# Optimization experiments

Measured on AMD Instinct MI355X. Metric: run time of the kernel, lower is better.

The kernel has to match this reference:

```python
import jax, jax.numpy as jnp
import numpy as np

EPS = 1e-12


def t5_layer_norm(x, w):
    # RMS norm without mean subtraction (T5 style)
    var = jnp.mean(x * x, axis=-1, keepdims=True)
    return w * (x * jax.lax.rsqrt(var + EPS))


def gether(h, a_simi, t_simi, adj):
    # h: [B,S,S,D]; a_simi/t_simi: [B,S]; adj: [B,S,S]
    diag = jnp.einsum('bssd->bsd', h)                 # h[b,l,l,:]
    h_adj = jnp.einsum('bld,blk->blkd', diag, adj)    # diag broadcast by adjacency
    h_y = h * t_simi[:, None, :, None]                # t_simi varies along axis 2
    h_x = h * a_simi[:, :, None, None]                # a_simi varies along axis 1
    h_left = jnp.pad(h_y, ((0, 0), (0, 0), (1, 0), (0, 0)))[:, :, :-1, :]
    h_right = jnp.pad(h_y, ((0, 0), (0, 0), (0, 1), (0, 0)))[:, :, 1:, :]
    h_up = jnp.pad(h_x, ((0, 0), (1, 0), (0, 0), (0, 0)))[:, :-1, :, :]
    h_down = jnp.pad(h_x, ((0, 0), (0, 1), (0, 0), (0, 0)))[:, 1:, :, :]
    return h + h_adj + h_left + h_right + h_up + h_down


def setup_inputs() -> dict:
    key = jax.random.key(0)
    ks = jax.random.split(key, 10)
    B, S, D_in, D_out = 8, 96, 768, 256
    table = jax.random.normal(ks[0], (B, S, S, D_in), dtype=jnp.float32)
    a_simi = jax.random.uniform(ks[1], (B, S), dtype=jnp.float32)
    t_simi = jax.random.uniform(ks[2], (B, S), dtype=jnp.float32)
    adj_matrix = jax.random.uniform(ks[3], (B, S, S), dtype=jnp.float32)
    s1 = 1.0 / np.sqrt(D_in)
    W1 = jax.random.uniform(ks[4], (D_in, D_in), jnp.float32, -s1, s1)
    b1 = jax.random.uniform(ks[5], (D_in,), jnp.float32, -s1, s1)
    g1 = jnp.ones((D_in,), jnp.float32)
    W2 = jax.random.uniform(ks[6], (D_in, D_out), jnp.float32, -s1, s1)
    b2 = jax.random.uniform(ks[7], (D_out,), jnp.float32, -s1, s1)
    g2 = jnp.ones((D_out,), jnp.float32)
    return {"table": table, "a_simi": a_simi, "t_simi": t_simi,
            "adj_matrix": adj_matrix, "W1": W1, "b1": b1, "g1": g1,
            "W2": W2, "b2": b2, "g2": g2}


def reference(table, a_simi, t_simi, adj_matrix, W1, b1, g1, W2, b2, g2):
    h0 = table
    h1 = gether(h0, a_simi, t_simi, adj_matrix)
    h1 = jax.nn.relu(t5_layer_norm((h1 + h0) @ W1 + b1, g1))
    h2 = gether(h1, a_simi, t_simi, adj_matrix)
    h2 = jax.nn.relu(t5_layer_norm((h2 + h1) @ W2 + b2, g2))
    return h2
```

## Files before the change

kernel.cpp:

```cpp
#include <hip/hip_runtime.h>

typedef __bf16 bf16;
typedef __bf16 bf16x4 __attribute__((ext_vector_type(4)));
typedef __bf16 bf16x8 __attribute__((ext_vector_type(8)));
typedef float f32x4 __attribute__((ext_vector_type(4)));
typedef float floatx4 __attribute__((ext_vector_type(4)));

#define S 96
#define DIN 768
#define DOUT 256
#define MROWS 73728

__device__ static inline void async16(const bf16* g, bf16* l) {
    __builtin_amdgcn_global_load_lds(
        (const __attribute__((address_space(1))) void*)g,
        (__attribute__((address_space(3))) void*)l,
        16, 0, 0);
}

__global__ __launch_bounds__(256) void k_gether1(
    const float* __restrict__ H, const float* __restrict__ Asim,
    const float* __restrict__ Tsim, const float* __restrict__ Adj,
    bf16* __restrict__ X)
{
    __shared__ float adjs[S];
    __shared__ float ts[S];
    __shared__ float diagf[DIN];
    int b = blockIdx.x / S, l = blockIdx.x % S;
    int tid = threadIdx.x;
    long row0 = (long)(b * S + l) * S;
    if (tid < S) {
        adjs[tid] = Adj[(b * S + l) * S + tid];
        ts[tid]   = Tsim[b * S + tid];
    }
    for (int i = tid; i < DIN / 4; i += 256)
        *(f32x4*)&diagf[i * 4] = *(const f32x4*)&H[(row0 + l) * DIN + i * 4];
    float a_up = (l > 0)     ? Asim[b * S + l - 1] : 0.f;
    float a_dn = (l < S - 1) ? Asim[b * S + l + 1] : 0.f;
    long du = (l > 0)     ? -(long)S * DIN : 0;
    long dd = (l < S - 1) ?  (long)S * DIN : 0;
    __syncthreads();

    for (int it = tid; it < S * (DIN / 4); it += 256) {
        int k = it / (DIN / 4);
        int c = it - k * (DIN / 4);
        const float* hc = H + (row0 + k) * DIN + c * 4;
        float tl = (k > 0)     ? ts[k - 1] : 0.f;
        float tr = (k < S - 1) ? ts[k + 1] : 0.f;
        long  dl = (k > 0)     ? -(long)DIN : 0;
        long  dr = (k < S - 1) ?  (long)DIN : 0;
        f32x4 vc = *(const f32x4*)hc;
        f32x4 vl = *(const f32x4*)(hc + dl);
        f32x4 vr = *(const f32x4*)(hc + dr);
        f32x4 vu = *(const f32x4*)(hc + du);
        f32x4 vd = *(const f32x4*)(hc + dd);
        float aj = adjs[k];
        bf16x4 o;
#pragma unroll
        for (int j = 0; j < 4; ++j) {
            float v = 2.f * vc[j] + aj * diagf[c * 4 + j]
                    + tl * vl[j] + tr * vr[j]
                    + a_up * vu[j] + a_dn * vd[j];
            o[j] = (bf16)v;
        }
        *(bf16x4*)&X[(row0 + k) * DIN + c * 4] = o;
    }
}

__global__ __launch_bounds__(256) void k_gether2(
    const bf16* __restrict__ Y, const float* __restrict__ INV,
    const float* __restrict__ G1, const float* __restrict__ Asim,
    const float* __restrict__ Tsim, const float* __restrict__ Adj,
    bf16* __restrict__ X)
{
    __shared__ float adjs[S];
    __shared__ float ts[S];
    __shared__ float diagf[DIN];
    __shared__ float g1s[DIN];
    int b = blockIdx.x / S, l = blockIdx.x % S;
    int tid = threadIdx.x;
    long row0 = (long)(b * S + l) * S;
    for (int i = tid; i < DIN; i += 256) g1s[i] = G1[i];
    __syncthreads();
    if (tid < S) {
        adjs[tid] = Adj[(b * S + l) * S + tid];
        ts[tid]   = Tsim[b * S + tid];
        float iv = INV[row0 + l];
        bf16x8 yv = *(const bf16x8*)&Y[(row0 + l) * DIN + tid * 8];
#pragma unroll
        for (int j = 0; j < 8; ++j) {
            float v = g1s[tid * 8 + j] * (float)yv[j] * iv;
            diagf[tid * 8 + j] = v > 0.f ? v : 0.f;
        }
    }
    float a_up = (l > 0)     ? Asim[b * S + l - 1] : 0.f;
    float a_dn = (l < S - 1) ? Asim[b * S + l + 1] : 0.f;
    long du = (l > 0)     ? -(long)S * DIN : 0;
    long dd = (l < S - 1) ?  (long)S * DIN : 0;
    int ou = (l > 0) ? -S : 0;
    int od = (l < S - 1) ? S : 0;
    __syncthreads();

    for (int it = tid; it < S * (DIN / 8); it += 256) {
        int k = it / (DIN / 8);
        int c = it - k * (DIN / 8);
        const bf16* yc = Y + (row0 + k) * DIN + c * 8;
        float tl = (k > 0)     ? ts[k - 1] : 0.f;
        float tr = (k < S - 1) ? ts[k + 1] : 0.f;
        int   ol = (k > 0)     ? -1 : 0;
        int   orr = (k < S - 1) ? 1 : 0;
        float ivc = INV[row0 + k];
        float ivl = INV[row0 + k + ol];
        float ivr = INV[row0 + k + orr];
        float ivu = INV[row0 + k + ou];
        float ivd = INV[row0 + k + od];
        bf16x8 vc = *(const bf16x8*)yc;
        bf16x8 vl = *(const bf16x8*)(yc + (long)ol * DIN);
        bf16x8 vr = *(const bf16x8*)(yc + (long)orr * DIN);
        bf16x8 vu = *(const bf16x8*)(yc + du);
        bf16x8 vd = *(const bf16x8*)(yc + dd);
        float aj = adjs[k];
        bf16x8 o;
#pragma unroll
        for (int j = 0; j < 8; ++j) {
            float g = g1s[c * 8 + j];
            float hc_ = g * (float)vc[j] * ivc; hc_ = hc_ > 0.f ? hc_ : 0.f;
            float hl_ = g * (float)vl[j] * ivl; hl_ = hl_ > 0.f ? hl_ : 0.f;
            float hr_ = g * (float)vr[j] * ivr; hr_ = hr_ > 0.f ? hr_ : 0.f;
            float hu_ = g * (float)vu[j] * ivu; hu_ = hu_ > 0.f ? hu_ : 0.f;
            float hd_ = g * (float)vd[j] * ivd; hd_ = hd_ > 0.f ? hd_ : 0.f;
            float v = 2.f * hc_ + aj * diagf[c * 8 + j]
                    + tl * hl_ + tr * hr_ + a_up * hu_ + a_dn * hd_;
            o[j] = (bf16)v;
        }
        *(bf16x8*)&X[(row0 + k) * DIN + c * 8] = o;
    }
}

template <int N, typename OutT>
__global__ __launch_bounds__(256) void k_gemm(
    const bf16* __restrict__ Xm, const bf16* __restrict__ WT,
    const float* __restrict__ bias, OutT* __restrict__ Y,
    float* __restrict__ ssq)
{
    constexpr int K = 768;
    __shared__ __align__(16) bf16 As[128 * 32];
    __shared__ __align__(16) bf16 Bs[128 * 32];
    int t = threadIdx.x;
    int colBase = blockIdx.x * 128;
    int rowBase = blockIdx.y * 128;
    int lane = t & 63, w = t >> 6;
    int quad = lane >> 4, l16 = lane & 15;
    int wr = w >> 1, wc = w & 1;

    floatx4 acc[4][4];
#pragma unroll
    for (int i = 0; i < 4; ++i)
#pragma unroll
        for (int j = 0; j < 4; ++j) acc[i][j] = (floatx4)0.f;

    const bf16* gA = Xm + (size_t)(rowBase + (t >> 2)) * K + (t & 3) * 8;
    const bf16* gB = WT + (size_t)(colBase + (t >> 2)) * K + (t & 3) * 8;
    bf16* ldsA = &As[t * 8];
    bf16* ldsB = &Bs[t * 8];

    for (int kk = 0; kk < K; kk += 32) {
        __syncthreads();
        async16(gA + kk, ldsA);
        async16(gA + kk + 64 * K, ldsA + 2048);
        async16(gB + kk, ldsB);
        async16(gB + kk + 64 * K, ldsB + 2048);
        __syncthreads();
        bf16x8 af[4], bfr[4];
#pragma unroll
        for (int i = 0; i < 4; ++i)
            af[i] = *(const bf16x8*)&As[(wr * 64 + i * 16 + l16) * 32 + quad * 8];
#pragma unroll
        for (int i = 0; i < 4; ++i)
            bfr[i] = *(const bf16x8*)&Bs[(wc * 64 + i * 16 + l16) * 32 + quad * 8];
#pragma unroll
        for (int i = 0; i < 4; ++i)
#pragma unroll
            for (int j = 0; j < 4; ++j)
                acc[i][j] = __builtin_amdgcn_mfma_f32_16x16x32_bf16(
                    af[i], bfr[j], acc[i][j], 0, 0, 0);
    }

    float bv[4];
#pragma unroll
    for (int j = 0; j < 4; ++j)
        bv[j] = bias[colBase + wc * 64 + j * 16 + l16];
#pragma unroll
    for (int i = 0; i < 4; ++i) {
#pragma unroll
        for (int r = 0; r < 4; ++r) {
            int row = rowBase + wr * 64 + i * 16 + quad * 4 + r;
            OutT* yp = Y + (size_t)row * N + colBase + wc * 64 + l16;
            float s = 0.f;
#pragma unroll
            for (int j = 0; j < 4; ++j) {
                float v = acc[i][j][r] + bv[j];
                s += v * v;
                yp[j * 16] = (OutT)v;
            }
            s += __shfl_xor(s, 1);
            s += __shfl_xor(s, 2);
            s += __shfl_xor(s, 4);
            s += __shfl_xor(s, 8);
            if (l16 == 0) atomicAdd(&ssq[row], s);
        }
    }
}

__global__ __launch_bounds__(256) void k_invr(float* ssq, int n, float invD)
{
    int i = blockIdx.x * 256 + threadIdx.x;
    if (i < n) ssq[i] = rsqrtf(ssq[i] * invD + 1e-12f);
}

__global__ __launch_bounds__(256) void k_final(
    const float* __restrict__ Y2, const float* __restrict__ ssq2,
    const float* __restrict__ G2, float* __restrict__ out)
{
    int gidx = blockIdx.x * 256 + threadIdx.x;
    int r = gidx >> 6;
    int c = (gidx & 63) * 4;
    float inv = rsqrtf(ssq2[r] * (1.f / DOUT) + 1e-12f);
    f32x4 yv = *(const f32x4*)&Y2[(size_t)r * DOUT + c];
    f32x4 o;
#pragma unroll
    for (int j = 0; j < 4; ++j) {
        float v = G2[c + j] * yv[j] * inv;
        o[j] = v > 0.f ? v : 0.f;
    }
    *(f32x4*)&out[(size_t)r * DOUT + c] = o;
}

__global__ __launch_bounds__(256) void k_castT(
    const float* __restrict__ in, bf16* __restrict__ out, int R, int C)
{
    int idx = blockIdx.x * 256 + threadIdx.x;
    if (idx < R * C) {
        int c = idx / R, r = idx - c * R;
        out[idx] = (bf16)in[r * C + c];
    }
}

extern "C" void kernel_launch(void* const* d_in, const int* in_sizes, int n_in,
                              void* d_out, int out_size, void* d_ws, size_t ws_size,
                              hipStream_t stream)
{
    const float* table = (const float*)d_in[0];
    const float* asim  = (const float*)d_in[1];
    const float* tsim  = (const float*)d_in[2];
    const float* adj   = (const float*)d_in[3];
    const float* W1    = (const float*)d_in[4];
    const float* b1    = (const float*)d_in[5];
    const float* g1    = (const float*)d_in[6];
    const float* W2    = (const float*)d_in[7];
    const float* b2    = (const float*)d_in[8];
    const float* g2    = (const float*)d_in[9];
    float* out = (float*)d_out;

    char* ws = (char*)d_ws;
    const size_t SZ_X = (size_t)MROWS * DIN * 2;
    bf16*  X    = (bf16*)ws;
    bf16*  Y1   = (bf16*)(ws + SZ_X);
    float* Y2   = (float*)(ws + SZ_X);
    bf16*  W1T  = (bf16*)(ws + 2 * SZ_X);
    bf16*  W2T  = (bf16*)(ws + 2 * SZ_X + 1179648);
    float* ssq1 = (float*)(ws + 2 * SZ_X + 1179648 + 393216);
    float* ssq2 = ssq1 + MROWS;

    hipMemsetAsync(ssq1, 0, (size_t)MROWS * 4 * 2, stream);
    k_castT<<<2304, 256, 0, stream>>>(W1, W1T, DIN, DIN);
    k_castT<<<768, 256, 0, stream>>>(W2, W2T, DIN, DOUT);

    k_gether1<<<8 * S, 256, 0, stream>>>(table, asim, tsim, adj, X);
    k_gemm<DIN, bf16><<<dim3(DIN / 128, MROWS / 128), 256, 0, stream>>>(X, W1T, b1, Y1, ssq1);
    k_invr<<<MROWS / 256, 256, 0, stream>>>(ssq1, MROWS, 1.f / DIN);
    k_gether2<<<8 * S, 256, 0, stream>>>(Y1, ssq1, g1, asim, tsim, adj, X);
    k_gemm<DOUT, float><<<dim3(DOUT / 128, MROWS / 128), 256, 0, stream>>>(X, W2T, b2, Y2, ssq2);
    k_final<<<(MROWS * DOUT / 4) / 256, 256, 0, stream>>>(Y2, ssq2, g2, out);
}
```

Baseline: 700.3 us.

## Restructure gether loops, load GEMM B from global, swizzle LDS, tiled transpose

The gether kernels now give each wavefront whole rows, with a fixed per-lane column unroll, instead of a flat index that needed a divide and modulo. The GEMM drops the LDS staging for the weight tile and loads B fragments straight from global memory (the weights are small and likely cached). It XOR-swizzles the A tile in LDS to cut bank conflicts, swaps the grid axes and adds an occupancy hint to launch bounds. The weight cast-transpose now goes through a padded shared-memory tile so reads and writes are coalesced. The risks are that the swapped grid order may reduce cache reuse of activation tiles across column blocks, and that per-wave global B loads add L2 traffic.

```diff
diff --git a/kernel.cpp b/kernel.cpp
--- a/kernel.cpp
+++ b/kernel.cpp
@@ -41,29 +41,34 @@
     long dd = (l < S - 1) ?  (long)S * DIN : 0;
     __syncthreads();
 
-    for (int it = tid; it < S * (DIN / 4); it += 256) {
-        int k = it / (DIN / 4);
-        int c = it - k * (DIN / 4);
-        const float* hc = H + (row0 + k) * DIN + c * 4;
+    int lane = tid & 63, wv = tid >> 6;
+    for (int k = wv; k < S; k += 4) {
         float tl = (k > 0)     ? ts[k - 1] : 0.f;
         float tr = (k < S - 1) ? ts[k + 1] : 0.f;
         long  dl = (k > 0)     ? -(long)DIN : 0;
         long  dr = (k < S - 1) ?  (long)DIN : 0;
-        f32x4 vc = *(const f32x4*)hc;
-        f32x4 vl = *(const f32x4*)(hc + dl);
-        f32x4 vr = *(const f32x4*)(hc + dr);
-        f32x4 vu = *(const f32x4*)(hc + du);
-        f32x4 vd = *(const f32x4*)(hc + dd);
         float aj = adjs[k];
-        bf16x4 o;
-#pragma unroll
-        for (int j = 0; j < 4; ++j) {
-            float v = 2.f * vc[j] + aj * diagf[c * 4 + j]
-                    + tl * vl[j] + tr * vr[j]
-                    + a_up * vu[j] + a_dn * vd[j];
-            o[j] = (bf16)v;
-        }
-        *(bf16x4*)&X[(row0 + k) * DIN + c * 4] = o;
+        const float* hrow = H + (row0 + k) * DIN;
+        bf16* xrow = X + (row0 + k) * DIN;
+#pragma unroll
+        for (int c = 0; c < 3; ++c) {
+            int col = (lane + c * 64) * 4;
+            const float* hc = hrow + col;
+            f32x4 vc = *(const f32x4*)hc;
+            f32x4 vl = *(const f32x4*)(hc + dl);
+            f32x4 vr = *(const f32x4*)(hc + dr);
+            f32x4 vu = *(const f32x4*)(hc + du);
+            f32x4 vd = *(const f32x4*)(hc + dd);
+            bf16x4 o;
+#pragma unroll
+            for (int j = 0; j < 4; ++j) {
+                float v = 2.f * vc[j] + aj * diagf[col + j]
+                        + tl * vl[j] + tr * vr[j]
+                        + a_up * vu[j] + a_dn * vd[j];
+                o[j] = (bf16)v;
+            }
+            *(bf16x4*)&xrow[col] = o;
+        }
     }
 }
 
@@ -101,54 +106,59 @@
     int od = (l < S - 1) ? S : 0;
     __syncthreads();
 
-    for (int it = tid; it < S * (DIN / 8); it += 256) {
-        int k = it / (DIN / 8);
-        int c = it - k * (DIN / 8);
-        const bf16* yc = Y + (row0 + k) * DIN + c * 8;
+    int lane = tid & 63, wv = tid >> 6;
+    for (int k = wv; k < S; k += 4) {
         float tl = (k > 0)     ? ts[k - 1] : 0.f;
         float tr = (k < S - 1) ? ts[k + 1] : 0.f;
         int   ol = (k > 0)     ? -1 : 0;
         int   orr = (k < S - 1) ? 1 : 0;
+        float aj = adjs[k];
         float ivc = INV[row0 + k];
         float ivl = INV[row0 + k + ol];
         float ivr = INV[row0 + k + orr];
         float ivu = INV[row0 + k + ou];
         float ivd = INV[row0 + k + od];
-        bf16x8 vc = *(const bf16x8*)yc;
-        bf16x8 vl = *(const bf16x8*)(yc + (long)ol * DIN);
-        bf16x8 vr = *(const bf16x8*)(yc + (long)orr * DIN);
-        bf16x8 vu = *(const bf16x8*)(yc + du);
-        bf16x8 vd = *(const bf16x8*)(yc + dd);
-        float aj = adjs[k];
-        bf16x8 o;
-#pragma unroll
-        for (int j = 0; j < 8; ++j) {
-            float g = g1s[c * 8 + j];
-            float hc_ = g * (float)vc[j] * ivc; hc_ = hc_ > 0.f ? hc_ : 0.f;
-            float hl_ = g * (float)vl[j] * ivl; hl_ = hl_ > 0.f ? hl_ : 0.f;
-            float hr_ = g * (float)vr[j] * ivr; hr_ = hr_ > 0.f ? hr_ : 0.f;
-            float hu_ = g * (float)vu[j] * ivu; hu_ = hu_ > 0.f ? hu_ : 0.f;
-            float hd_ = g * (float)vd[j] * ivd; hd_ = hd_ > 0.f ? hd_ : 0.f;
-            float v = 2.f * hc_ + aj * diagf[c * 8 + j]
-                    + tl * hl_ + tr * hr_ + a_up * hu_ + a_dn * hd_;
-            o[j] = (bf16)v;
-        }
-        *(bf16x8*)&X[(row0 + k) * DIN + c * 8] = o;
+        const bf16* yrow = Y + (row0 + k) * DIN;
+        bf16* xrow = X + (row0 + k) * DIN;
+#pragma unroll
+        for (int c2 = 0; c2 < 2; ++c2) {
+            int col = (lane + c2 * 64) * 8;
+            if (col >= DIN) break;
+            const bf16* yc = yrow + col;
+            bf16x8 vc = *(const bf16x8*)yc;
+            bf16x8 vl = *(const bf16x8*)(yc + (long)ol * DIN);
+            bf16x8 vr = *(const bf16x8*)(yc + (long)orr * DIN);
+            bf16x8 vu = *(const bf16x8*)(yc + du);
+            bf16x8 vd = *(const bf16x8*)(yc + dd);
+            bf16x8 o;
+#pragma unroll
+            for (int j = 0; j < 8; ++j) {
+                float g = g1s[col + j];
+                float hc_ = g * (float)vc[j] * ivc; hc_ = hc_ > 0.f ? hc_ : 0.f;
+                float hl_ = g * (float)vl[j] * ivl; hl_ = hl_ > 0.f ? hl_ : 0.f;
+                float hr_ = g * (float)vr[j] * ivr; hr_ = hr_ > 0.f ? hr_ : 0.f;
+                float hu_ = g * (float)vu[j] * ivu; hu_ = hu_ > 0.f ? hu_ : 0.f;
+                float hd_ = g * (float)vd[j] * ivd; hd_ = hd_ > 0.f ? hd_ : 0.f;
+                float v = 2.f * hc_ + aj * diagf[col + j]
+                        + tl * hl_ + tr * hr_ + a_up * hu_ + a_dn * hd_;
+                o[j] = (bf16)v;
+            }
+            *(bf16x8*)&xrow[col] = o;
+        }
     }
 }
 
 template <int N, typename OutT>
-__global__ __launch_bounds__(256) void k_gemm(
+__global__ __launch_bounds__(256, 3) void k_gemm(
     const bf16* __restrict__ Xm, const bf16* __restrict__ WT,
     const float* __restrict__ bias, OutT* __restrict__ Y,
     float* __restrict__ ssq)
 {
     constexpr int K = 768;
     __shared__ __align__(16) bf16 As[128 * 32];
-    __shared__ __align__(16) bf16 Bs[128 * 32];
     int t = threadIdx.x;
-    int colBase = blockIdx.x * 128;
-    int rowBase = blockIdx.y * 128;
+    int rowBase = blockIdx.x * 128;
+    int colBase = blockIdx.y * 128;
     int lane = t & 63, w = t >> 6;
     int quad = lane >> 4, l16 = lane & 15;
     int wr = w >> 1, wc = w & 1;
@@ -159,25 +169,26 @@
 #pragma unroll
         for (int j = 0; j < 4; ++j) acc[i][j] = (floatx4)0.f;
 
-    const bf16* gA = Xm + (size_t)(rowBase + (t >> 2)) * K + (t & 3) * 8;
-    const bf16* gB = WT + (size_t)(colBase + (t >> 2)) * K + (t & 3) * 8;
+    int chunk = (t & 3) ^ ((t >> 3) & 3);
+    const bf16* gA = Xm + (size_t)(rowBase + (t >> 2)) * K + chunk * 8;
     bf16* ldsA = &As[t * 8];
-    bf16* ldsB = &Bs[t * 8];
+    const bf16* gB = WT + (size_t)(colBase + wc * 64 + l16) * K + quad * 8;
 
     for (int kk = 0; kk < K; kk += 32) {
+        bf16x8 bfr[4];
+#pragma unroll
+        for (int j = 0; j < 4; ++j)
+            bfr[j] = *(const bf16x8*)(gB + (size_t)(j * 16) * K + kk);
         __syncthreads();
         async16(gA + kk, ldsA);
         async16(gA + kk + 64 * K, ldsA + 2048);
-        async16(gB + kk, ldsB);
-        async16(gB + kk + 64 * K, ldsB + 2048);
         __syncthreads();
-        bf16x8 af[4], bfr[4];
-#pragma unroll
-        for (int i = 0; i < 4; ++i)
-            af[i] = *(const bf16x8*)&As[(wr * 64 + i * 16 + l16) * 32 + quad * 8];
-#pragma unroll
-        for (int i = 0; i < 4; ++i)
-            bfr[i] = *(const bf16x8*)&Bs[(wc * 64 + i * 16 + l16) * 32 + quad * 8];
+        bf16x8 af[4];
+#pragma unroll
+        for (int i = 0; i < 4; ++i) {
+            int ra = wr * 64 + i * 16 + l16;
+            af[i] = *(const bf16x8*)&As[ra * 32 + (quad ^ ((ra >> 1) & 3)) * 8];
+        }
 #pragma unroll
         for (int i = 0; i < 4; ++i)
 #pragma unroll
@@ -239,11 +250,16 @@
 __global__ __launch_bounds__(256) void k_castT(
     const float* __restrict__ in, bf16* __restrict__ out, int R, int C)
 {
-    int idx = blockIdx.x * 256 + threadIdx.x;
-    if (idx < R * C) {
-        int c = idx / R, r = idx - c * R;
-        out[idx] = (bf16)in[r * C + c];
-    }
+    __shared__ float tile[32][33];
+    int lx = threadIdx.x & 31, ly = threadIdx.x >> 5;
+    int c0 = blockIdx.x * 32, r0 = blockIdx.y * 32;
+#pragma unroll
+    for (int k = 0; k < 4; ++k)
+        tile[ly + 8 * k][lx] = in[(size_t)(r0 + ly + 8 * k) * C + c0 + lx];
+    __syncthreads();
+#pragma unroll
+    for (int k = 0; k < 4; ++k)
+        out[(size_t)(c0 + ly + 8 * k) * R + r0 + lx] = (bf16)tile[lx][ly + 8 * k];
 }
 
 extern "C" void kernel_launch(void* const* d_in, const int* in_sizes, int n_in,
@@ -273,13 +289,13 @@
     float* ssq2 = ssq1 + MROWS;
 
     hipMemsetAsync(ssq1, 0, (size_t)MROWS * 4 * 2, stream);
-    k_castT<<<2304, 256, 0, stream>>>(W1, W1T, DIN, DIN);
-    k_castT<<<768, 256, 0, stream>>>(W2, W2T, DIN, DOUT);
+    k_castT<<<dim3(DIN / 32, DIN / 32), 256, 0, stream>>>(W1, W1T, DIN, DIN);
+    k_castT<<<dim3(DOUT / 32, DIN / 32), 256, 0, stream>>>(W2, W2T, DIN, DOUT);
 
     k_gether1<<<8 * S, 256, 0, stream>>>(table, asim, tsim, adj, X);
-    k_gemm<DIN, bf16><<<dim3(DIN / 128, MROWS / 128), 256, 0, stream>>>(X, W1T, b1, Y1, ssq1);
+    k_gemm<DIN, bf16><<<dim3(MROWS / 128, DIN / 128), 256, 0, stream>>>(X, W1T, b1, Y1, ssq1);
     k_invr<<<MROWS / 256, 256, 0, stream>>>(ssq1, MROWS, 1.f / DIN);
     k_gether2<<<8 * S, 256, 0, stream>>>(Y1, ssq1, g1, asim, tsim, adj, X);
-    k_gemm<DOUT, float><<<dim3(DOUT / 128, MROWS / 128), 256, 0, stream>>>(X, W2T, b2, Y2, ssq2);
+    k_gemm<DOUT, float><<<dim3(MROWS / 128, DOUT / 128), 256, 0, stream>>>(X, W2T, b2, Y2, ssq2);
     k_final<<<(MROWS * DOUT / 4) / 256, 256, 0, stream>>>(Y2, ssq2, g2, out);
 }
```

Result: slower. 773.1 us (+10.4%).
